# Kernel tuning notes

Measured on AMD Instinct MI355X. Metric: run time of the kernel, lower is better.

Reference implementation:

```python
import jax, jax.numpy as jnp
import numpy as np

D = 64          # d_in
NH = [256, 256] # nn_depth_design
L = 16          # flow_layers
B = 32768       # batch of samples


def _build_masks():
    # Deterministic mask maps: this_min=0, this_max=d_in-1 for all layers
    mh0 = np.arange(NH[0]) % (D - 1)
    mh1 = np.arange(NH[1]) % (D - 1)
    M1 = (mh0[None, :] <= mh1[:, None]).astype(np.float32)  # [nh1, nh0]
    M0s, M2s = [], []
    for l in range(L):
        perm = np.arange(D) if l % 2 == 0 else np.arange(D)[::-1]
        M0s.append((perm[None, :] <= mh0[:, None]).astype(np.float32))  # [nh0, D]
        M2s.append((mh1[None, :] < perm[:, None]).astype(np.float32))  # [D, nh1]
    M0 = np.stack(M0s)                                   # [L, nh0, D]
    M1 = np.broadcast_to(M1, (L,) + M1.shape).copy()     # [L, nh1, nh0]
    M2 = np.stack(M2s)                                   # [L, D, nh1]
    return jnp.asarray(M0), jnp.asarray(M1), jnp.asarray(M2)


def setup_inputs() -> dict:
    key = jax.random.key(0)
    ks = jax.random.split(key, 13)
    u = jax.random.normal(ks[0], (B, D), dtype=jnp.float32)

    def w(k, shape, fan_in):
        return jax.random.uniform(k, shape, jnp.float32, -1.0, 1.0) / np.sqrt(fan_in)

    inp = {"u": u}
    i = 1
    for net in ("loc", "scale"):
        inp[f"{net}_W0"] = w(ks[i], (L, NH[0], D), D); i += 1
        inp[f"{net}_b0"] = w(ks[i], (L, NH[0]), D); i += 1
        inp[f"{net}_W1"] = w(ks[i], (L, NH[1], NH[0]), NH[0]); i += 1
        inp[f"{net}_b1"] = w(ks[i], (L, NH[1]), NH[0]); i += 1
        inp[f"{net}_W2"] = w(ks[i], (L, D, NH[1]), NH[1]); i += 1
        inp[f"{net}_b2"] = w(ks[i], (L, D), NH[1]); i += 1
    M0, M1, M2 = _build_masks()
    inp["M0"], inp["M1"], inp["M2"] = M0, M1, M2
    return inp


def reference(u, loc_W0, loc_b0, loc_W1, loc_b1, loc_W2, loc_b2,
              scale_W0, scale_b0, scale_W1, scale_b1, scale_W2, scale_b2,
              M0, M1, M2):
    def step(y, p):
        (lW0, lb0, lW1, lb1, lW2, lb2,
         sW0, sb0, sW1, sb1, sW2, sb2, m0, m1, m2) = p

        def net(W0, b0, W1, b1, W2, b2):
            h = jax.nn.relu(y @ (m0 * W0).T + b0)    # [B, nh0]
            h = jax.nn.relu(h @ (m1 * W1).T + b1)    # [B, nh1]
            return h @ (m2 * W2).T + b2              # [B, D]

        loc = net(lW0, lb0, lW1, lb1, lW2, lb2)
        sc = net(sW0, sb0, sW1, sb1, sW2, sb2)
        # inverse=False coupling: exp(-scale) * (y - loc)
        return jnp.exp(-sc) * (y - loc), None

    params = (loc_W0, loc_b0, loc_W1, loc_b1, loc_W2, loc_b2,
              scale_W0, scale_b0, scale_W1, scale_b1, scale_W2, scale_b2,
              M0, M1, M2)
    y, _ = jax.lax.scan(step, u, params)
    return y
```

## Files before the change

### kernel.cpp

```cpp
#include <hip/hip_runtime.h>
#include <hip/hip_bf16.h>

typedef __bf16 bf16x8 __attribute__((ext_vector_type(8)));
typedef float  f32x4  __attribute__((ext_vector_type(4)));

#define LAYERS 16
#define DIM 64
#define NHID 256
#define BATCH 32768
#define MTILE 64
#define NBLOCKS (BATCH / MTILE)

#define W0P_PER 16384
#define W1P_PER 65536
#define W2P_PER 16384
#define W0P_TOT (32 * W0P_PER)
#define W1P_TOT (32 * W1P_PER)
#define W2P_TOT (32 * W2P_PER)
#define PACK_TOT (W0P_TOT + W1P_TOT + W2P_TOT)

__global__ __launch_bounds__(256) void pack_weights(
    const float* __restrict__ lW0, const float* __restrict__ lW1, const float* __restrict__ lW2,
    const float* __restrict__ sW0, const float* __restrict__ sW1, const float* __restrict__ sW2,
    const float* __restrict__ M0,  const float* __restrict__ M1,  const float* __restrict__ M2,
    __bf16* __restrict__ ws)
{
    const long i = ((long)blockIdx.x * 256 + threadIdx.x) * 8;
    const float* W; const float* M; long src;
    if (i < W0P_TOT) {
        int netl = (int)(i / W0P_PER), rem = (int)(i % W0P_PER);
        int net = netl >> 4, l = netl & 15;
        int nt = rem >> 10, kt = (rem >> 9) & 1, lane = (rem >> 3) & 63;
        int n = nt * 16 + (lane & 15), k = kt * 32 + (lane >> 4) * 8;
        W = net ? sW0 : lW0; M = M0;
        src = (long)(l * 256 + n) * 64 + k;
    } else if (i < W0P_TOT + W1P_TOT) {
        long r = i - W0P_TOT;
        int netl = (int)(r / W1P_PER), rem = (int)(r % W1P_PER);
        int net = netl >> 4, l = netl & 15;
        int nt = rem >> 12, kt = (rem >> 9) & 7, lane = (rem >> 3) & 63;
        int n = nt * 16 + (lane & 15), k = kt * 32 + (lane >> 4) * 8;
        W = net ? sW1 : lW1; M = M1;
        src = (long)(l * 256 + n) * 256 + k;
    } else {
        long r = i - W0P_TOT - W1P_TOT;
        int netl = (int)(r / W2P_PER), rem = (int)(r % W2P_PER);
        int net = netl >> 4, l = netl & 15;
        int nt = rem >> 12, kt = (rem >> 9) & 7, lane = (rem >> 3) & 63;
        int n = nt * 16 + (lane & 15), k = kt * 32 + (lane >> 4) * 8;
        W = net ? sW2 : lW2; M = M2;
        src = (long)(l * 64 + n) * 256 + k;
    }
    f32x4 wa = *(const f32x4*)(W + src);
    f32x4 wb = *(const f32x4*)(W + src + 4);
    f32x4 ma = *(const f32x4*)(M + src);
    f32x4 mb = *(const f32x4*)(M + src + 4);
    bf16x8 o;
    o[0] = (__bf16)(wa[0] * ma[0]); o[1] = (__bf16)(wa[1] * ma[1]);
    o[2] = (__bf16)(wa[2] * ma[2]); o[3] = (__bf16)(wa[3] * ma[3]);
    o[4] = (__bf16)(wb[0] * mb[0]); o[5] = (__bf16)(wb[1] * mb[1]);
    o[6] = (__bf16)(wb[2] * mb[2]); o[7] = (__bf16)(wb[3] * mb[3]);
    *(bf16x8*)(ws + i) = o;
}

__global__ __launch_bounds__(256, 2) void flow_kernel(
    const float* __restrict__ u,
    const __bf16* __restrict__ wp,
    const float* __restrict__ lb0, const float* __restrict__ lb1, const float* __restrict__ lb2,
    const float* __restrict__ sb0, const float* __restrict__ sb1, const float* __restrict__ sb2,
    float* __restrict__ out)
{
    __shared__ __bf16 ybf[MTILE][72];
    __shared__ __bf16 buf1[MTILE][264];
    __shared__ __bf16 buf2[MTILE][264];

    const int tid  = threadIdx.x;
    const int wave = tid >> 6;
    const int lane = tid & 63;
    const int quad = lane >> 4;
    const int l16  = lane & 15;
    const int blk  = blockIdx.x;

    const __bf16* w0p = wp;
    const __bf16* w1p = wp + W0P_TOT;
    const __bf16* w2p = wp + W0P_TOT + W1P_TOT;

    float y[4][4];
    #pragma unroll
    for (int mt = 0; mt < 4; ++mt)
        #pragma unroll
        for (int r = 0; r < 4; ++r) {
            int row = blk * MTILE + mt * 16 + quad * 4 + r;
            y[mt][r] = u[row * DIM + wave * 16 + l16];
        }

    for (int l = 0; l < LAYERS; ++l) {
        #pragma unroll
        for (int mt = 0; mt < 4; ++mt)
            #pragma unroll
            for (int r = 0; r < 4; ++r)
                ybf[mt * 16 + quad * 4 + r][wave * 16 + l16] = (__bf16)y[mt][r];
        __syncthreads();

        float locr[4][4], scr[4][4];

        #pragma unroll
        for (int net = 0; net < 2; ++net) {
            const __bf16* w0b = w0p + (long)(net * 16 + l) * W0P_PER;
            const __bf16* w1b = w1p + (long)(net * 16 + l) * W1P_PER;
            const __bf16* w2b = w2p + (long)(net * 16 + l) * W2P_PER;
            const float* b0 = (net ? sb0 : lb0) + l * 256;
            const float* b1 = (net ? sb1 : lb1) + l * 256;
            const float* b2 = (net ? sb2 : lb2) + l * 64;

            {
                f32x4 acc[4][4];
                #pragma unroll
                for (int mt = 0; mt < 4; ++mt)
                    #pragma unroll
                    for (int nt = 0; nt < 4; ++nt)
                        acc[mt][nt] = (f32x4){0.f, 0.f, 0.f, 0.f};
                #pragma unroll
                for (int kt = 0; kt < 2; ++kt) {
                    bf16x8 a[4], b[4];
                    #pragma unroll
                    for (int mt = 0; mt < 4; ++mt)
                        a[mt] = *(const bf16x8*)&ybf[mt * 16 + l16][kt * 32 + quad * 8];
                    #pragma unroll
                    for (int nt = 0; nt < 4; ++nt)
                        b[nt] = *(const bf16x8*)(w0b + (long)((wave * 4 + nt) * 2 + kt) * 512 + lane * 8);
                    #pragma unroll
                    for (int mt = 0; mt < 4; ++mt)
                        #pragma unroll
                        for (int nt = 0; nt < 4; ++nt)
                            acc[mt][nt] = __builtin_amdgcn_mfma_f32_16x16x32_bf16(a[mt], b[nt], acc[mt][nt], 0, 0, 0);
                }
                #pragma unroll
                for (int nt = 0; nt < 4; ++nt) {
                    float bias = b0[(wave * 4 + nt) * 16 + l16];
                    #pragma unroll
                    for (int mt = 0; mt < 4; ++mt)
                        #pragma unroll
                        for (int r = 0; r < 4; ++r) {
                            float v = acc[mt][nt][r] + bias;
                            buf1[mt * 16 + quad * 4 + r][(wave * 4 + nt) * 16 + l16] = (__bf16)fmaxf(v, 0.f);
                        }
                }
            }
            __syncthreads();

            {
                f32x4 acc[4][4];
                #pragma unroll
                for (int mt = 0; mt < 4; ++mt)
                    #pragma unroll
                    for (int nt = 0; nt < 4; ++nt)
                        acc[mt][nt] = (f32x4){0.f, 0.f, 0.f, 0.f};
                #pragma unroll
                for (int kt = 0; kt < 8; ++kt) {
                    bf16x8 a[4], b[4];
                    #pragma unroll
                    for (int mt = 0; mt < 4; ++mt)
                        a[mt] = *(const bf16x8*)&buf1[mt * 16 + l16][kt * 32 + quad * 8];
                    #pragma unroll
                    for (int nt = 0; nt < 4; ++nt)
                        b[nt] = *(const bf16x8*)(w1b + (long)((wave * 4 + nt) * 8 + kt) * 512 + lane * 8);
                    #pragma unroll
                    for (int mt = 0; mt < 4; ++mt)
                        #pragma unroll
                        for (int nt = 0; nt < 4; ++nt)
                            acc[mt][nt] = __builtin_amdgcn_mfma_f32_16x16x32_bf16(a[mt], b[nt], acc[mt][nt], 0, 0, 0);
                }
                #pragma unroll
                for (int nt = 0; nt < 4; ++nt) {
                    float bias = b1[(wave * 4 + nt) * 16 + l16];
                    #pragma unroll
                    for (int mt = 0; mt < 4; ++mt)
                        #pragma unroll
                        for (int r = 0; r < 4; ++r) {
                            float v = acc[mt][nt][r] + bias;
                            buf2[mt * 16 + quad * 4 + r][(wave * 4 + nt) * 16 + l16] = (__bf16)fmaxf(v, 0.f);
                        }
                }
            }
            __syncthreads();

            {
                f32x4 acc[4];
                #pragma unroll
                for (int mt = 0; mt < 4; ++mt)
                    acc[mt] = (f32x4){0.f, 0.f, 0.f, 0.f};
                #pragma unroll
                for (int kt = 0; kt < 8; ++kt) {
                    bf16x8 a[4];
                    bf16x8 b = *(const bf16x8*)(w2b + (long)(wave * 8 + kt) * 512 + lane * 8);
                    #pragma unroll
                    for (int mt = 0; mt < 4; ++mt)
                        a[mt] = *(const bf16x8*)&buf2[mt * 16 + l16][kt * 32 + quad * 8];
                    #pragma unroll
                    for (int mt = 0; mt < 4; ++mt)
                        acc[mt] = __builtin_amdgcn_mfma_f32_16x16x32_bf16(a[mt], b, acc[mt], 0, 0, 0);
                }
                float bias = b2[wave * 16 + l16];
                if (net == 0) {
                    #pragma unroll
                    for (int mt = 0; mt < 4; ++mt)
                        #pragma unroll
                        for (int r = 0; r < 4; ++r)
                            locr[mt][r] = acc[mt][r] + bias;
                } else {
                    #pragma unroll
                    for (int mt = 0; mt < 4; ++mt)
                        #pragma unroll
                        for (int r = 0; r < 4; ++r)
                            scr[mt][r] = acc[mt][r] + bias;
                }
            }
        }

        #pragma unroll
        for (int mt = 0; mt < 4; ++mt)
            #pragma unroll
            for (int r = 0; r < 4; ++r)
                y[mt][r] = __expf(-scr[mt][r]) * (y[mt][r] - locr[mt][r]);
    }

    #pragma unroll
    for (int mt = 0; mt < 4; ++mt)
        #pragma unroll
        for (int r = 0; r < 4; ++r) {
            int row = blk * MTILE + mt * 16 + quad * 4 + r;
            out[row * DIM + wave * 16 + l16] = y[mt][r];
        }
}

extern "C" void kernel_launch(void* const* d_in, const int* in_sizes, int n_in,
                              void* d_out, int out_size, void* d_ws, size_t ws_size,
                              hipStream_t stream) {
    const float* u   = (const float*)d_in[0];
    const float* lW0 = (const float*)d_in[1];
    const float* lb0 = (const float*)d_in[2];
    const float* lW1 = (const float*)d_in[3];
    const float* lb1 = (const float*)d_in[4];
    const float* lW2 = (const float*)d_in[5];
    const float* lb2 = (const float*)d_in[6];
    const float* sW0 = (const float*)d_in[7];
    const float* sb0 = (const float*)d_in[8];
    const float* sW1 = (const float*)d_in[9];
    const float* sb1 = (const float*)d_in[10];
    const float* sW2 = (const float*)d_in[11];
    const float* sb2 = (const float*)d_in[12];
    const float* M0  = (const float*)d_in[13];
    const float* M1  = (const float*)d_in[14];
    const float* M2  = (const float*)d_in[15];

    if (ws_size < (size_t)PACK_TOT * sizeof(__bf16)) return;
    __bf16* ws = (__bf16*)d_ws;

    pack_weights<<<PACK_TOT / 8 / 256, 256, 0, stream>>>(
        lW0, lW1, lW2, sW0, sW1, sW2, M0, M1, M2, ws);
    flow_kernel<<<NBLOCKS, 256, 0, stream>>>(
        u, ws, lb0, lb1, lb2, sb0, sb1, sb2, (float*)d_out);
}
```

Baseline: 347.9 us.

## Use 512-thread blocks with transposed MFMA operands and vectorized LDS/global stores

Doubles the threads per block to eight waves, each computing half the hidden tiles. The MFMA operands are swapped so weights are the A operand and activations the B operand, which yields a transposed accumulator layout. That layout allows 4-wide bf16 LDS stores, vector bias loads, and f32x4 global loads and stores of y. The aim is more latency hiding per block with fewer accumulator registers per wave, at the cost of more waves sharing the same barriers.

```diff
diff --git a/kernel.cpp b/kernel.cpp
--- a/kernel.cpp
+++ b/kernel.cpp
@@ -2,6 +2,7 @@
 #include <hip/hip_bf16.h>
 
 typedef __bf16 bf16x8 __attribute__((ext_vector_type(8)));
+typedef __bf16 bf16x4 __attribute__((ext_vector_type(4)));
 typedef float  f32x4  __attribute__((ext_vector_type(4)));
 
 #define LAYERS 16
@@ -63,7 +64,7 @@
     *(bf16x8*)(ws + i) = o;
 }
 
-__global__ __launch_bounds__(256, 2) void flow_kernel(
+__global__ __launch_bounds__(512, 4) void flow_kernel(
     const float* __restrict__ u,
     const __bf16* __restrict__ wp,
     const float* __restrict__ lb0, const float* __restrict__ lb1, const float* __restrict__ lb2,
@@ -81,28 +82,35 @@
     const int l16  = lane & 15;
     const int blk  = blockIdx.x;
 
+    const int whid = wave * 2;
+    const int mt3  = wave >> 1;
+    const int ntb  = (wave & 1) * 2;
+
     const __bf16* w0p = wp;
     const __bf16* w1p = wp + W0P_TOT;
     const __bf16* w2p = wp + W0P_TOT + W1P_TOT;
 
-    float y[4][4];
+    float y[2][4];
     #pragma unroll
-    for (int mt = 0; mt < 4; ++mt)
-        #pragma unroll
-        for (int r = 0; r < 4; ++r) {
-            int row = blk * MTILE + mt * 16 + quad * 4 + r;
-            y[mt][r] = u[row * DIM + wave * 16 + l16];
+    for (int ntl = 0; ntl < 2; ++ntl) {
+        const float* src = u + (long)(blk * MTILE + (ntb + ntl) * 16 + l16) * DIM
+                             + mt3 * 16 + quad * 4;
+        f32x4 t = *(const f32x4*)src;
+        #pragma unroll
+        for (int r = 0; r < 4; ++r) y[ntl][r] = t[r];
+    }
+
+    for (int l = 0; l < LAYERS; ++l) {
+        #pragma unroll
+        for (int ntl = 0; ntl < 2; ++ntl) {
+            bf16x4 v;
+            #pragma unroll
+            for (int r = 0; r < 4; ++r) v[r] = (__bf16)y[ntl][r];
+            *(bf16x4*)&ybf[(ntb + ntl) * 16 + l16][mt3 * 16 + quad * 4] = v;
         }
-
-    for (int l = 0; l < LAYERS; ++l) {
-        #pragma unroll
-        for (int mt = 0; mt < 4; ++mt)
-            #pragma unroll
-            for (int r = 0; r < 4; ++r)
-                ybf[mt * 16 + quad * 4 + r][wave * 16 + l16] = (__bf16)y[mt][r];
         __syncthreads();
 
-        float locr[4][4], scr[4][4];
+        float locr[2][4], scr[2][4];
 
         #pragma unroll
         for (int net = 0; net < 2; ++net) {
@@ -114,124 +122,125 @@
             const float* b2 = (net ? sb2 : lb2) + l * 64;
 
             {
-                f32x4 acc[4][4];
-                #pragma unroll
-                for (int mt = 0; mt < 4; ++mt)
+                f32x4 acc[2][4];
+                #pragma unroll
+                for (int mt = 0; mt < 2; ++mt)
                     #pragma unroll
                     for (int nt = 0; nt < 4; ++nt)
                         acc[mt][nt] = (f32x4){0.f, 0.f, 0.f, 0.f};
                 #pragma unroll
                 for (int kt = 0; kt < 2; ++kt) {
-                    bf16x8 a[4], b[4];
-                    #pragma unroll
-                    for (int mt = 0; mt < 4; ++mt)
-                        a[mt] = *(const bf16x8*)&ybf[mt * 16 + l16][kt * 32 + quad * 8];
-                    #pragma unroll
-                    for (int nt = 0; nt < 4; ++nt)
-                        b[nt] = *(const bf16x8*)(w0b + (long)((wave * 4 + nt) * 2 + kt) * 512 + lane * 8);
-                    #pragma unroll
-                    for (int mt = 0; mt < 4; ++mt)
+                    bf16x8 aw[2], bv[4];
+                    #pragma unroll
+                    for (int mt = 0; mt < 2; ++mt)
+                        aw[mt] = *(const bf16x8*)(w0b + (long)((whid + mt) * 2 + kt) * 512 + lane * 8);
+                    #pragma unroll
+                    for (int nt = 0; nt < 4; ++nt)
+                        bv[nt] = *(const bf16x8*)&ybf[nt * 16 + l16][kt * 32 + quad * 8];
+                    #pragma unroll
+                    for (int mt = 0; mt < 2; ++mt)
                         #pragma unroll
                         for (int nt = 0; nt < 4; ++nt)
-                            acc[mt][nt] = __builtin_amdgcn_mfma_f32_16x16x32_bf16(a[mt], b[nt], acc[mt][nt], 0, 0, 0);
-                }
-                #pragma unroll
-                for (int nt = 0; nt < 4; ++nt) {
-                    float bias = b0[(wave * 4 + nt) * 16 + l16];
-                    #pragma unroll
-                    for (int mt = 0; mt < 4; ++mt)
-                        #pragma unroll
-                        for (int r = 0; r < 4; ++r) {
-                            float v = acc[mt][nt][r] + bias;
-                            buf1[mt * 16 + quad * 4 + r][(wave * 4 + nt) * 16 + l16] = (__bf16)fmaxf(v, 0.f);
-                        }
+                            acc[mt][nt] = __builtin_amdgcn_mfma_f32_16x16x32_bf16(aw[mt], bv[nt], acc[mt][nt], 0, 0, 0);
+                }
+                #pragma unroll
+                for (int mt = 0; mt < 2; ++mt) {
+                    f32x4 bias = *(const f32x4*)(b0 + (whid + mt) * 16 + quad * 4);
+                    #pragma unroll
+                    for (int nt = 0; nt < 4; ++nt) {
+                        bf16x4 v;
+                        #pragma unroll
+                        for (int r = 0; r < 4; ++r)
+                            v[r] = (__bf16)fmaxf(acc[mt][nt][r] + bias[r], 0.f);
+                        *(bf16x4*)&buf1[nt * 16 + l16][(whid + mt) * 16 + quad * 4] = v;
+                    }
                 }
             }
             __syncthreads();
 
             {
-                f32x4 acc[4][4];
-                #pragma unroll
-                for (int mt = 0; mt < 4; ++mt)
+                f32x4 acc[2][4];
+                #pragma unroll
+                for (int mt = 0; mt < 2; ++mt)
                     #pragma unroll
                     for (int nt = 0; nt < 4; ++nt)
                         acc[mt][nt] = (f32x4){0.f, 0.f, 0.f, 0.f};
                 #pragma unroll
                 for (int kt = 0; kt < 8; ++kt) {
-                    bf16x8 a[4], b[4];
-                    #pragma unroll
-                    for (int mt = 0; mt < 4; ++mt)
-                        a[mt] = *(const bf16x8*)&buf1[mt * 16 + l16][kt * 32 + quad * 8];
-                    #pragma unroll
-                    for (int nt = 0; nt < 4; ++nt)
-                        b[nt] = *(const bf16x8*)(w1b + (long)((wave * 4 + nt) * 8 + kt) * 512 + lane * 8);
-                    #pragma unroll
-                    for (int mt = 0; mt < 4; ++mt)
+                    bf16x8 aw[2], bv[4];
+                    #pragma unroll
+                    for (int mt = 0; mt < 2; ++mt)
+                        aw[mt] = *(const bf16x8*)(w1b + (long)((whid + mt) * 8 + kt) * 512 + lane * 8);
+                    #pragma unroll
+                    for (int nt = 0; nt < 4; ++nt)
+                        bv[nt] = *(const bf16x8*)&buf1[nt * 16 + l16][kt * 32 + quad * 8];
+                    #pragma unroll
+                    for (int mt = 0; mt < 2; ++mt)
                         #pragma unroll
                         for (int nt = 0; nt < 4; ++nt)
-                            acc[mt][nt] = __builtin_amdgcn_mfma_f32_16x16x32_bf16(a[mt], b[nt], acc[mt][nt], 0, 0, 0);
-                }
-                #pragma unroll
-                for (int nt = 0; nt < 4; ++nt) {
-                    float bias = b1[(wave * 4 + nt) * 16 + l16];
-                    #pragma unroll
-                    for (int mt = 0; mt < 4; ++mt)
-                        #pragma unroll
-                        for (int r = 0; r < 4; ++r) {
-                            float v = acc[mt][nt][r] + bias;
-                            buf2[mt * 16 + quad * 4 + r][(wave * 4 + nt) * 16 + l16] = (__bf16)fmaxf(v, 0.f);
-                        }
+                            acc[mt][nt] = __builtin_amdgcn_mfma_f32_16x16x32_bf16(aw[mt], bv[nt], acc[mt][nt], 0, 0, 0);
+                }
+                #pragma unroll
+                for (int mt = 0; mt < 2; ++mt) {
+                    f32x4 bias = *(const f32x4*)(b1 + (whid + mt) * 16 + quad * 4);
+                    #pragma unroll
+                    for (int nt = 0; nt < 4; ++nt) {
+                        bf16x4 v;
+                        #pragma unroll
+                        for (int r = 0; r < 4; ++r)
+                            v[r] = (__bf16)fmaxf(acc[mt][nt][r] + bias[r], 0.f);
+                        *(bf16x4*)&buf2[nt * 16 + l16][(whid + mt) * 16 + quad * 4] = v;
+                    }
                 }
             }
             __syncthreads();
 
             {
-                f32x4 acc[4];
-                #pragma unroll
-                for (int mt = 0; mt < 4; ++mt)
-                    acc[mt] = (f32x4){0.f, 0.f, 0.f, 0.f};
+                f32x4 acc[2];
+                acc[0] = (f32x4){0.f, 0.f, 0.f, 0.f};
+                acc[1] = (f32x4){0.f, 0.f, 0.f, 0.f};
                 #pragma unroll
                 for (int kt = 0; kt < 8; ++kt) {
-                    bf16x8 a[4];
-                    bf16x8 b = *(const bf16x8*)(w2b + (long)(wave * 8 + kt) * 512 + lane * 8);
-                    #pragma unroll
-                    for (int mt = 0; mt < 4; ++mt)
-                        a[mt] = *(const bf16x8*)&buf2[mt * 16 + l16][kt * 32 + quad * 8];
-                    #pragma unroll
-                    for (int mt = 0; mt < 4; ++mt)
-                        acc[mt] = __builtin_amdgcn_mfma_f32_16x16x32_bf16(a[mt], b, acc[mt], 0, 0, 0);
-                }
-                float bias = b2[wave * 16 + l16];
+                    bf16x8 aw = *(const bf16x8*)(w2b + (long)(mt3 * 8 + kt) * 512 + lane * 8);
+                    #pragma unroll
+                    for (int ntl = 0; ntl < 2; ++ntl) {
+                        bf16x8 bv = *(const bf16x8*)&buf2[(ntb + ntl) * 16 + l16][kt * 32 + quad * 8];
+                        acc[ntl] = __builtin_amdgcn_mfma_f32_16x16x32_bf16(aw, bv, acc[ntl], 0, 0, 0);
+                    }
+                }
+                f32x4 bias = *(const f32x4*)(b2 + mt3 * 16 + quad * 4);
                 if (net == 0) {
                     #pragma unroll
-                    for (int mt = 0; mt < 4; ++mt)
-                        #pragma unroll
-                        for (int r = 0; r < 4; ++r)
-                            locr[mt][r] = acc[mt][r] + bias;
+                    for (int ntl = 0; ntl < 2; ++ntl)
+                        #pragma unroll
+                        for (int r = 0; r < 4; ++r)
+                            locr[ntl][r] = acc[ntl][r] + bias[r];
                 } else {
                     #pragma unroll
-                    for (int mt = 0; mt < 4; ++mt)
-                        #pragma unroll
-                        for (int r = 0; r < 4; ++r)
-                            scr[mt][r] = acc[mt][r] + bias;
+                    for (int ntl = 0; ntl < 2; ++ntl)
+                        #pragma unroll
+                        for (int r = 0; r < 4; ++r)
+                            scr[ntl][r] = acc[ntl][r] + bias[r];
                 }
             }
         }
 
         #pragma unroll
-        for (int mt = 0; mt < 4; ++mt)
+        for (int ntl = 0; ntl < 2; ++ntl)
             #pragma unroll
             for (int r = 0; r < 4; ++r)
-                y[mt][r] = __expf(-scr[mt][r]) * (y[mt][r] - locr[mt][r]);
+                y[ntl][r] = __expf(-scr[ntl][r]) * (y[ntl][r] - locr[ntl][r]);
     }
 
     #pragma unroll
-    for (int mt = 0; mt < 4; ++mt)
-        #pragma unroll
-        for (int r = 0; r < 4; ++r) {
-            int row = blk * MTILE + mt * 16 + quad * 4 + r;
-            out[row * DIM + wave * 16 + l16] = y[mt][r];
-        }
+    for (int ntl = 0; ntl < 2; ++ntl) {
+        f32x4 t;
+        #pragma unroll
+        for (int r = 0; r < 4; ++r) t[r] = y[ntl][r];
+        float* dst = out + (long)(blk * MTILE + (ntb + ntl) * 16 + l16) * DIM
+                         + mt3 * 16 + quad * 4;
+        *(f32x4*)dst = t;
+    }
 }
 
 extern "C" void kernel_launch(void* const* d_in, const int* in_sizes, int n_in,
@@ -259,6 +268,6 @@
 
     pack_weights<<<PACK_TOT / 8 / 256, 256, 0, stream>>>(
         lW0, lW1, lW2, sW0, sW1, sW2, M0, M1, M2, ws);
-    flow_kernel<<<NBLOCKS, 256, 0, stream>>>(
+    flow_kernel<<<NBLOCKS, 512, 0, stream>>>(
         u, ws, lb0, lb1, lb2, sb0, sb1, sb2, (float*)d_out);
 }
```

After: 369.7 us. +6.2%, slower.

## Swap MFMA operands and prefetch next-stage weights into registers

Applied to the files above, without the earlier changes.

Swaps the MFMA operand roles so weights become the A operand and activations the B operand. This transposes the accumulator layout, which allows vectorized bf16x4 LDS stores, f32x4 bias loads and f32x4 global loads and stores of y. It also software-prefetches the next stage's weights into registers (the first W1 k-tiles, all of W2, and the next net or layer's W0) before the epilogue and barrier, to hide global load latency. The cost is higher register pressure under launch_bounds(256,2), which could cause spills.

```diff
diff --git a/kernel.cpp b/kernel.cpp
--- a/kernel.cpp
+++ b/kernel.cpp
@@ -2,6 +2,7 @@
 #include <hip/hip_bf16.h>
 
 typedef __bf16 bf16x8 __attribute__((ext_vector_type(8)));
+typedef __bf16 bf16x4 __attribute__((ext_vector_type(4)));
 typedef float  f32x4  __attribute__((ext_vector_type(4)));
 
 #define LAYERS 16
@@ -18,6 +19,8 @@
 #define W1P_TOT (32 * W1P_PER)
 #define W2P_TOT (32 * W2P_PER)
 #define PACK_TOT (W0P_TOT + W1P_TOT + W2P_TOT)
+
+__device__ __forceinline__ bf16x8 ldw(const __bf16* p) { return *(const bf16x8*)p; }
 
 __global__ __launch_bounds__(256) void pack_weights(
     const float* __restrict__ lW0, const float* __restrict__ lW1, const float* __restrict__ lW2,
@@ -63,7 +66,8 @@
     *(bf16x8*)(ws + i) = o;
 }
 
-__global__ __launch_bounds__(256, 2) void flow_kernel(
+__global__ void __launch_bounds__(256, 2)
+flow_kernel(
     const float* __restrict__ u,
     const __bf16* __restrict__ wp,
     const float* __restrict__ lb0, const float* __restrict__ lb1, const float* __restrict__ lb2,
@@ -85,102 +89,121 @@
     const __bf16* w1p = wp + W0P_TOT;
     const __bf16* w2p = wp + W0P_TOT + W1P_TOT;
 
-    float y[4][4];
+    f32x4 y[4];
     #pragma unroll
-    for (int mt = 0; mt < 4; ++mt)
-        #pragma unroll
-        for (int r = 0; r < 4; ++r) {
-            int row = blk * MTILE + mt * 16 + quad * 4 + r;
-            y[mt][r] = u[row * DIM + wave * 16 + l16];
+    for (int bt = 0; bt < 4; ++bt)
+        y[bt] = *(const f32x4*)(u + (long)(blk * MTILE + bt * 16 + l16) * DIM
+                                  + wave * 16 + quad * 4);
+
+    bf16x8 wg1[8];
+    #pragma unroll
+    for (int ot = 0; ot < 4; ++ot)
+        #pragma unroll
+        for (int kt = 0; kt < 2; ++kt)
+            wg1[ot * 2 + kt] = ldw(w0p + (long)((4 * wave + ot) * 2 + kt) * 512 + lane * 8);
+
+    for (int l = 0; l < LAYERS; ++l) {
+        #pragma unroll
+        for (int bt = 0; bt < 4; ++bt) {
+            bf16x4 v;
+            #pragma unroll
+            for (int r = 0; r < 4; ++r) v[r] = (__bf16)y[bt][r];
+            *(bf16x4*)&ybf[bt * 16 + l16][wave * 16 + quad * 4] = v;
         }
-
-    for (int l = 0; l < LAYERS; ++l) {
-        #pragma unroll
-        for (int mt = 0; mt < 4; ++mt)
-            #pragma unroll
-            for (int r = 0; r < 4; ++r)
-                ybf[mt * 16 + quad * 4 + r][wave * 16 + l16] = (__bf16)y[mt][r];
         __syncthreads();
 
-        float locr[4][4], scr[4][4];
+        f32x4 locr[4], scr[4];
 
         #pragma unroll
         for (int net = 0; net < 2; ++net) {
-            const __bf16* w0b = w0p + (long)(net * 16 + l) * W0P_PER;
             const __bf16* w1b = w1p + (long)(net * 16 + l) * W1P_PER;
             const __bf16* w2b = w2p + (long)(net * 16 + l) * W2P_PER;
+            const __bf16* w0n = w0p + (long)(net == 0 ? 16 + l : l + 1) * W0P_PER;
             const float* b0 = (net ? sb0 : lb0) + l * 256;
             const float* b1 = (net ? sb1 : lb1) + l * 256;
             const float* b2 = (net ? sb2 : lb2) + l * 64;
 
+            bf16x8 wg2a[8];
+
             {
                 f32x4 acc[4][4];
                 #pragma unroll
-                for (int mt = 0; mt < 4; ++mt)
-                    #pragma unroll
-                    for (int nt = 0; nt < 4; ++nt)
-                        acc[mt][nt] = (f32x4){0.f, 0.f, 0.f, 0.f};
+                for (int ot = 0; ot < 4; ++ot)
+                    #pragma unroll
+                    for (int bt = 0; bt < 4; ++bt)
+                        acc[ot][bt] = (f32x4){0.f, 0.f, 0.f, 0.f};
                 #pragma unroll
                 for (int kt = 0; kt < 2; ++kt) {
-                    bf16x8 a[4], b[4];
-                    #pragma unroll
-                    for (int mt = 0; mt < 4; ++mt)
-                        a[mt] = *(const bf16x8*)&ybf[mt * 16 + l16][kt * 32 + quad * 8];
-                    #pragma unroll
-                    for (int nt = 0; nt < 4; ++nt)
-                        b[nt] = *(const bf16x8*)(w0b + (long)((wave * 4 + nt) * 2 + kt) * 512 + lane * 8);
-                    #pragma unroll
-                    for (int mt = 0; mt < 4; ++mt)
-                        #pragma unroll
-                        for (int nt = 0; nt < 4; ++nt)
-                            acc[mt][nt] = __builtin_amdgcn_mfma_f32_16x16x32_bf16(a[mt], b[nt], acc[mt][nt], 0, 0, 0);
-                }
-                #pragma unroll
-                for (int nt = 0; nt < 4; ++nt) {
-                    float bias = b0[(wave * 4 + nt) * 16 + l16];
-                    #pragma unroll
-                    for (int mt = 0; mt < 4; ++mt)
-                        #pragma unroll
-                        for (int r = 0; r < 4; ++r) {
-                            float v = acc[mt][nt][r] + bias;
-                            buf1[mt * 16 + quad * 4 + r][(wave * 4 + nt) * 16 + l16] = (__bf16)fmaxf(v, 0.f);
-                        }
+                    bf16x8 bv[4];
+                    #pragma unroll
+                    for (int bt = 0; bt < 4; ++bt)
+                        bv[bt] = *(const bf16x8*)&ybf[bt * 16 + l16][kt * 32 + quad * 8];
+                    #pragma unroll
+                    for (int ot = 0; ot < 4; ++ot)
+                        #pragma unroll
+                        for (int bt = 0; bt < 4; ++bt)
+                            acc[ot][bt] = __builtin_amdgcn_mfma_f32_16x16x32_bf16(wg1[ot * 2 + kt], bv[bt], acc[ot][bt], 0, 0, 0);
+                }
+                #pragma unroll
+                for (int kt = 0; kt < 2; ++kt)
+                    #pragma unroll
+                    for (int ot = 0; ot < 4; ++ot)
+                        wg2a[kt * 4 + ot] = ldw(w1b + (long)((4 * wave + ot) * 8 + kt) * 512 + lane * 8);
+                #pragma unroll
+                for (int ot = 0; ot < 4; ++ot) {
+                    f32x4 bias = *(const f32x4*)(b0 + (4 * wave + ot) * 16 + quad * 4);
+                    #pragma unroll
+                    for (int bt = 0; bt < 4; ++bt) {
+                        bf16x4 v;
+                        #pragma unroll
+                        for (int r = 0; r < 4; ++r)
+                            v[r] = (__bf16)fmaxf(acc[ot][bt][r] + bias[r], 0.f);
+                        *(bf16x4*)&buf1[bt * 16 + l16][(4 * wave + ot) * 16 + quad * 4] = v;
+                    }
                 }
             }
             __syncthreads();
 
+            bf16x8 wg3[8];
+
             {
                 f32x4 acc[4][4];
                 #pragma unroll
-                for (int mt = 0; mt < 4; ++mt)
-                    #pragma unroll
-                    for (int nt = 0; nt < 4; ++nt)
-                        acc[mt][nt] = (f32x4){0.f, 0.f, 0.f, 0.f};
+                for (int ot = 0; ot < 4; ++ot)
+                    #pragma unroll
+                    for (int bt = 0; bt < 4; ++bt)
+                        acc[ot][bt] = (f32x4){0.f, 0.f, 0.f, 0.f};
                 #pragma unroll
                 for (int kt = 0; kt < 8; ++kt) {
-                    bf16x8 a[4], b[4];
-                    #pragma unroll
-                    for (int mt = 0; mt < 4; ++mt)
-                        a[mt] = *(const bf16x8*)&buf1[mt * 16 + l16][kt * 32 + quad * 8];
-                    #pragma unroll
-                    for (int nt = 0; nt < 4; ++nt)
-                        b[nt] = *(const bf16x8*)(w1b + (long)((wave * 4 + nt) * 8 + kt) * 512 + lane * 8);
-                    #pragma unroll
-                    for (int mt = 0; mt < 4; ++mt)
-                        #pragma unroll
-                        for (int nt = 0; nt < 4; ++nt)
-                            acc[mt][nt] = __builtin_amdgcn_mfma_f32_16x16x32_bf16(a[mt], b[nt], acc[mt][nt], 0, 0, 0);
-                }
-                #pragma unroll
-                for (int nt = 0; nt < 4; ++nt) {
-                    float bias = b1[(wave * 4 + nt) * 16 + l16];
-                    #pragma unroll
-                    for (int mt = 0; mt < 4; ++mt)
-                        #pragma unroll
-                        for (int r = 0; r < 4; ++r) {
-                            float v = acc[mt][nt][r] + bias;
-                            buf2[mt * 16 + quad * 4 + r][(wave * 4 + nt) * 16 + l16] = (__bf16)fmaxf(v, 0.f);
-                        }
+                    bf16x8 aw[4];
+                    #pragma unroll
+                    for (int ot = 0; ot < 4; ++ot)
+                        aw[ot] = (kt < 2) ? wg2a[kt * 4 + ot]
+                                          : ldw(w1b + (long)((4 * wave + ot) * 8 + kt) * 512 + lane * 8);
+                    bf16x8 bv[4];
+                    #pragma unroll
+                    for (int bt = 0; bt < 4; ++bt)
+                        bv[bt] = *(const bf16x8*)&buf1[bt * 16 + l16][kt * 32 + quad * 8];
+                    #pragma unroll
+                    for (int ot = 0; ot < 4; ++ot)
+                        #pragma unroll
+                        for (int bt = 0; bt < 4; ++bt)
+                            acc[ot][bt] = __builtin_amdgcn_mfma_f32_16x16x32_bf16(aw[ot], bv[bt], acc[ot][bt], 0, 0, 0);
+                }
+                #pragma unroll
+                for (int kt = 0; kt < 8; ++kt)
+                    wg3[kt] = ldw(w2b + (long)(wave * 8 + kt) * 512 + lane * 8);
+                #pragma unroll
+                for (int ot = 0; ot < 4; ++ot) {
+                    f32x4 bias = *(const f32x4*)(b1 + (4 * wave + ot) * 16 + quad * 4);
+                    #pragma unroll
+                    for (int bt = 0; bt < 4; ++bt) {
+                        bf16x4 v;
+                        #pragma unroll
+                        for (int r = 0; r < 4; ++r)
+                            v[r] = (__bf16)fmaxf(acc[ot][bt][r] + bias[r], 0.f);
+                        *(bf16x4*)&buf2[bt * 16 + l16][(4 * wave + ot) * 16 + quad * 4] = v;
+                    }
                 }
             }
             __syncthreads();
@@ -188,50 +211,49 @@
             {
                 f32x4 acc[4];
                 #pragma unroll
-                for (int mt = 0; mt < 4; ++mt)
-                    acc[mt] = (f32x4){0.f, 0.f, 0.f, 0.f};
+                for (int bt = 0; bt < 4; ++bt)
+                    acc[bt] = (f32x4){0.f, 0.f, 0.f, 0.f};
                 #pragma unroll
                 for (int kt = 0; kt < 8; ++kt) {
-                    bf16x8 a[4];
-                    bf16x8 b = *(const bf16x8*)(w2b + (long)(wave * 8 + kt) * 512 + lane * 8);
-                    #pragma unroll
-                    for (int mt = 0; mt < 4; ++mt)
-                        a[mt] = *(const bf16x8*)&buf2[mt * 16 + l16][kt * 32 + quad * 8];
-                    #pragma unroll
-                    for (int mt = 0; mt < 4; ++mt)
-                        acc[mt] = __builtin_amdgcn_mfma_f32_16x16x32_bf16(a[mt], b, acc[mt], 0, 0, 0);
-                }
-                float bias = b2[wave * 16 + l16];
+                    #pragma unroll
+                    for (int bt = 0; bt < 4; ++bt) {
+                        bf16x8 bv = *(const bf16x8*)&buf2[bt * 16 + l16][kt * 32 + quad * 8];
+                        acc[bt] = __builtin_amdgcn_mfma_f32_16x16x32_bf16(wg3[kt], bv, acc[bt], 0, 0, 0);
+                    }
+                }
+                #pragma unroll
+                for (int ot = 0; ot < 4; ++ot)
+                    #pragma unroll
+                    for (int kt = 0; kt < 2; ++kt)
+                        wg1[ot * 2 + kt] = ldw(w0n + (long)((4 * wave + ot) * 2 + kt) * 512 + lane * 8);
+                f32x4 bias = *(const f32x4*)(b2 + wave * 16 + quad * 4);
                 if (net == 0) {
                     #pragma unroll
-                    for (int mt = 0; mt < 4; ++mt)
-                        #pragma unroll
-                        for (int r = 0; r < 4; ++r)
-                            locr[mt][r] = acc[mt][r] + bias;
+                    for (int bt = 0; bt < 4; ++bt)
+                        #pragma unroll
+                        for (int r = 0; r < 4; ++r)
+                            locr[bt][r] = acc[bt][r] + bias[r];
                 } else {
                     #pragma unroll
-                    for (int mt = 0; mt < 4; ++mt)
-                        #pragma unroll
-                        for (int r = 0; r < 4; ++r)
-                            scr[mt][r] = acc[mt][r] + bias;
+                    for (int bt = 0; bt < 4; ++bt)
+                        #pragma unroll
+                        for (int r = 0; r < 4; ++r)
+                            scr[bt][r] = acc[bt][r] + bias[r];
                 }
             }
         }
 
         #pragma unroll
-        for (int mt = 0; mt < 4; ++mt)
+        for (int bt = 0; bt < 4; ++bt)
             #pragma unroll
             for (int r = 0; r < 4; ++r)
-                y[mt][r] = __expf(-scr[mt][r]) * (y[mt][r] - locr[mt][r]);
+                y[bt][r] = __expf(-scr[bt][r]) * (y[bt][r] - locr[bt][r]);
     }
 
     #pragma unroll
-    for (int mt = 0; mt < 4; ++mt)
-        #pragma unroll
-        for (int r = 0; r < 4; ++r) {
-            int row = blk * MTILE + mt * 16 + quad * 4 + r;
-            out[row * DIM + wave * 16 + l16] = y[mt][r];
-        }
+    for (int bt = 0; bt < 4; ++bt)
+        *(f32x4*)(out + (long)(blk * MTILE + bt * 16 + l16) * DIM
+                      + wave * 16 + quad * 4) = y[bt];
 }
 
 extern "C" void kernel_launch(void* const* d_in, const int* in_sizes, int n_in,
```

Measured after the change: 317.2 us. 1.1x faster.
